# Kernel tuning notes

Measured on AMD Instinct MI355X. Metric: run time of the kernel, lower is better.

Reference implementation:

```python
import jax, jax.numpy as jnp
import numpy as np


def setup_inputs() -> dict:
    key = jax.random.key(0)
    qkv = jax.random.normal(key, (8, 1536, 2048), dtype=jnp.float32)
    return {"qkv": qkv, "n_heads": 8}


def reference(qkv, n_heads):
    # qkv: [N, H*3*C, T] -> output [N, H*C, T]
    bs, width, length = qkv.shape
    assert width % (3 * n_heads) == 0
    ch = width // (3 * n_heads)
    qkv_r = qkv.reshape(bs * n_heads, 3 * ch, length)
    q, k, v = qkv_r[:, :ch], qkv_r[:, ch:2 * ch], qkv_r[:, 2 * ch:]
    scale = 1.0 / np.sqrt(np.sqrt(ch))  # applied to both q and k
    # [B, T, S] scores
    weight = jnp.einsum('bct,bcs->bts', q * scale, k * scale)
    weight = jax.nn.softmax(weight.astype(jnp.float32), axis=-1).astype(weight.dtype)
    a = jnp.einsum('bts,bcs->bct', weight, v)
    return a.reshape(bs, n_heads * ch, length)
```

## Files before the change

kernel.cpp:

```cpp
#include <hip/hip_runtime.h>


typedef __bf16 bf16;
typedef __bf16 bf16x4 __attribute__((ext_vector_type(4)));
typedef __bf16 bf16x8 __attribute__((ext_vector_type(8)));
typedef float  f32x4  __attribute__((ext_vector_type(4)));
typedef float  f32x16 __attribute__((ext_vector_type(16)));
typedef unsigned int u32;

#define NLEN 2048
#define DCH  64
#define HSTR (NLEN * DCH * 2)
#define WS_K (16u * 1024u * 1024u)
#define WS_V (32u * 1024u * 1024u)
#define WS_NEED (48u * 1024u * 1024u)
#define PSCALE 0.42466119f

__device__ __forceinline__ int swzK(int row, int cb) {
    return row * 128 + ((((cb >> 4) ^ row) & 7) << 4) + (cb & 15);
}
__device__ __forceinline__ int swzO(int row, int cb) {
    int g = cb >> 4;
    g = (g & ~7) | ((g ^ row) & 7);
    return row * 512 + (g << 4) + (cb & 15);
}

__device__ __forceinline__ void gload16(const char* g, char* l) {
    __builtin_amdgcn_global_load_lds((const __attribute__((address_space(1))) void*)g,
                                     (__attribute__((address_space(3))) void*)l, 16, 0, 0);
}

__global__ __launch_bounds__(256)
void prep(const float* __restrict__ qkv, char* __restrict__ ws)
{
    const int tid  = threadIdx.x;
    const int pb   = blockIdx.x;
    const int head = blockIdx.y;
    const int type = blockIdx.z;

    const float* src = qkv + (size_t)head * (3 * DCH) * NLEN + (size_t)type * DCH * NLEN;
    char* dst = ws + (type == 0 ? 0u : (type == 1 ? WS_K : WS_V))
                   + (size_t)head * HSTR + (size_t)pb * 8192;

    if (type < 2) {
        __shared__ float T[64][65];
        #pragma unroll
        for (int p = 0; p < 4; ++p) {
            int idx = tid + p * 256;
            int c = idx >> 4, q4 = idx & 15;
            float4 f = *(const float4*)(src + (size_t)c * NLEN + pb * 64 + q4 * 4);
            T[q4 * 4 + 0][c] = f.x * PSCALE;
            T[q4 * 4 + 1][c] = f.y * PSCALE;
            T[q4 * 4 + 2][c] = f.z * PSCALE;
            T[q4 * 4 + 3][c] = f.w * PSCALE;
        }
        __syncthreads();
        #pragma unroll
        for (int p = 0; p < 2; ++p) {
            int gidx = tid + p * 256;
            int s = gidx >> 3, G = gidx & 7;
            int c0 = (G ^ (s & 7)) * 8;
            bf16 tmp[8];
            #pragma unroll
            for (int j = 0; j < 8; ++j) tmp[j] = (bf16)T[s][c0 + j];
            *(bf16x8*)(dst + s * 128 + G * 16) = *(bf16x8*)tmp;
        }
    } else {
        const int c = tid >> 2, so = (tid & 3) * 16;
        const float* sp = src + (size_t)c * NLEN + pb * 64 + so;
        float f[16];
        #pragma unroll
        for (int j = 0; j < 4; ++j) *(f32x4*)(f + 4 * j) = *(const f32x4*)(sp + 4 * j);
        #pragma unroll
        for (int gl = 0; gl < 2; ++gl) {
            bf16 tmp[8];
            #pragma unroll
            for (int j = 0; j < 8; ++j) tmp[j] = (bf16)f[gl * 8 + j];
            const int Gp = ((so >> 3) + gl) ^ (c & 7);
            *(bf16x8*)(dst + c * 128 + Gp * 16) = *(bf16x8*)tmp;
        }
    }
}

__global__ __launch_bounds__(256, 2)
void attn_main(const char* __restrict__ ws, float* __restrict__ out)
{
    const int tid  = threadIdx.x;
    const int lane = tid & 63;
    const int w    = tid >> 6;
    const int hi   = lane >> 5;
    const int ll5  = lane & 31;

    const int bid  = blockIdx.x;
    const int head = (bid & 7) * 8 + ((bid >> 3) & 7);
    const int tblk = bid >> 6;
    const int t0   = tblk * 256;

    const char* Qb = ws + (size_t)head * HSTR + (size_t)t0 * 128;
    const char* Kb = ws + WS_K + (size_t)head * HSTR;
    const char* Vb = ws + WS_V + (size_t)head * HSTR;

    __shared__ __align__(16) char lds[32768];

    #pragma unroll
    for (int i = 0; i < 8; ++i)
        gload16(Qb + tid * 16 + i * 4096, lds + tid * 16 + i * 4096);
    asm volatile("s_waitcnt vmcnt(0)");
    __syncthreads();

    bf16x8 qf0[4], qf1[4];
    #pragma unroll
    for (int kc = 0; kc < 4; ++kc) {
        qf0[kc] = *(const bf16x8*)(lds + swzK(w * 64 + ll5,      kc * 32 + hi * 16));
        qf1[kc] = *(const bf16x8*)(lds + swzK(w * 64 + 32 + ll5, kc * 32 + hi * 16));
    }
    __syncthreads();

    gload16(Kb + tid * 16,        lds + tid * 16);
    gload16(Kb + 4096 + tid * 16, lds + 4096 + tid * 16);
    gload16(Vb + tid * 16,        lds + 8192 + tid * 16);
    gload16(Vb + 4096 + tid * 16, lds + 12288 + tid * 16);
    asm volatile("s_waitcnt vmcnt(0)");
    __syncthreads();

    f32x16 o00 = {}, o01 = {}, o10 = {}, o11 = {};
    float l0 = 0.f, l1 = 0.f;
    int cur = 0;

    for (int sb = 0; sb < 32; ++sb) {
        if (sb < 31) {
            char* bn = lds + (cur ^ 1) * 16384;
            const char* kn = Kb + (size_t)(sb + 1) * 8192;
            const char* vn = Vb + (size_t)(sb + 1) * 8192;
            gload16(kn + tid * 16,        bn + tid * 16);
            gload16(kn + 4096 + tid * 16, bn + 4096 + tid * 16);
            gload16(vn + tid * 16,        bn + 8192 + tid * 16);
            gload16(vn + 4096 + tid * 16, bn + 12288 + tid * 16);
        }
        char* Kc = lds + cur * 16384;
        char* Vc = Kc + 8192;

        f32x16 s00 = {}, s10 = {}, s01 = {}, s11 = {};
        __builtin_amdgcn_s_setprio(1);
        #pragma unroll
        for (int kc = 0; kc < 4; ++kc) {
            bf16x8 a0 = *(const bf16x8*)(Kc + swzK(ll5,      kc * 32 + hi * 16));
            bf16x8 a1 = *(const bf16x8*)(Kc + swzK(32 + ll5, kc * 32 + hi * 16));
            s00 = __builtin_amdgcn_mfma_f32_32x32x16_bf16(a0, qf0[kc], s00, 0, 0, 0);
            s10 = __builtin_amdgcn_mfma_f32_32x32x16_bf16(a1, qf0[kc], s10, 0, 0, 0);
            s01 = __builtin_amdgcn_mfma_f32_32x32x16_bf16(a0, qf1[kc], s01, 0, 0, 0);
            s11 = __builtin_amdgcn_mfma_f32_32x32x16_bf16(a1, qf1[kc], s11, 0, 0, 0);
        }
        __builtin_amdgcn_s_setprio(0);

        {
            float a = 0.f, b = 0.f, c = 0.f, d = 0.f;
            #pragma unroll
            for (int r = 0; r < 16; r += 4) {
                s00[r+0] = __builtin_amdgcn_exp2f(s00[r+0]); a += s00[r+0];
                s00[r+1] = __builtin_amdgcn_exp2f(s00[r+1]); b += s00[r+1];
                s00[r+2] = __builtin_amdgcn_exp2f(s00[r+2]); c += s00[r+2];
                s00[r+3] = __builtin_amdgcn_exp2f(s00[r+3]); d += s00[r+3];
            }
            #pragma unroll
            for (int r = 0; r < 16; r += 4) {
                s10[r+0] = __builtin_amdgcn_exp2f(s10[r+0]); a += s10[r+0];
                s10[r+1] = __builtin_amdgcn_exp2f(s10[r+1]); b += s10[r+1];
                s10[r+2] = __builtin_amdgcn_exp2f(s10[r+2]); c += s10[r+2];
                s10[r+3] = __builtin_amdgcn_exp2f(s10[r+3]); d += s10[r+3];
            }
            l0 += (a + b) + (c + d);
        }
        {
            float a = 0.f, b = 0.f, c = 0.f, d = 0.f;
            #pragma unroll
            for (int r = 0; r < 16; r += 4) {
                s01[r+0] = __builtin_amdgcn_exp2f(s01[r+0]); a += s01[r+0];
                s01[r+1] = __builtin_amdgcn_exp2f(s01[r+1]); b += s01[r+1];
                s01[r+2] = __builtin_amdgcn_exp2f(s01[r+2]); c += s01[r+2];
                s01[r+3] = __builtin_amdgcn_exp2f(s01[r+3]); d += s01[r+3];
            }
            #pragma unroll
            for (int r = 0; r < 16; r += 4) {
                s11[r+0] = __builtin_amdgcn_exp2f(s11[r+0]); a += s11[r+0];
                s11[r+1] = __builtin_amdgcn_exp2f(s11[r+1]); b += s11[r+1];
                s11[r+2] = __builtin_amdgcn_exp2f(s11[r+2]); c += s11[r+2];
                s11[r+3] = __builtin_amdgcn_exp2f(s11[r+3]); d += s11[r+3];
            }
            l1 += (a + b) + (c + d);
        }

        bf16x8 pa0[4], pa1[4];
        #pragma unroll
        for (int th = 0; th < 2; ++th) {
            const f32x16& sl = th ? s01 : s00;
            const f32x16& sh = th ? s11 : s10;
            bf16x8* pa = th ? pa1 : pa0;
            #pragma unroll
            for (int ks = 0; ks < 4; ++ks) {
                const f32x16& pp = (ks < 2) ? sl : sh;
                const int rb = (ks & 1) * 8;
                u32 X, X2, Y, Y2;
                asm("v_cvt_pk_bf16_f32 %0, %1, %2" : "=v"(X)  : "v"(pp[rb + 0]), "v"(pp[rb + 1]));
                asm("v_cvt_pk_bf16_f32 %0, %1, %2" : "=v"(X2) : "v"(pp[rb + 2]), "v"(pp[rb + 3]));
                asm("v_cvt_pk_bf16_f32 %0, %1, %2" : "=v"(Y)  : "v"(pp[rb + 4]), "v"(pp[rb + 5]));
                asm("v_cvt_pk_bf16_f32 %0, %1, %2" : "=v"(Y2) : "v"(pp[rb + 6]), "v"(pp[rb + 7]));
                asm("v_permlane32_swap_b32 %0, %1" : "+v"(X),  "+v"(Y));
                asm("v_permlane32_swap_b32 %0, %1" : "+v"(X2), "+v"(Y2));
                u32 wds[4] = {X, X2, Y, Y2};
                pa[ks] = *(bf16x8*)wds;
            }
        }

        __builtin_amdgcn_s_setprio(1);
        #pragma unroll
        for (int ks = 0; ks < 4; ++ks) {
            bf16x8 b0 = *(const bf16x8*)(Vc + swzK(ll5,      ks * 32 + hi * 16));
            bf16x8 b1 = *(const bf16x8*)(Vc + swzK(32 + ll5, ks * 32 + hi * 16));
            o00 = __builtin_amdgcn_mfma_f32_32x32x16_bf16(pa0[ks], b0, o00, 0, 0, 0);
            o01 = __builtin_amdgcn_mfma_f32_32x32x16_bf16(pa0[ks], b1, o01, 0, 0, 0);
            o10 = __builtin_amdgcn_mfma_f32_32x32x16_bf16(pa1[ks], b0, o10, 0, 0, 0);
            o11 = __builtin_amdgcn_mfma_f32_32x32x16_bf16(pa1[ks], b1, o11, 0, 0, 0);
        }
        __builtin_amdgcn_s_setprio(0);

        asm volatile("s_waitcnt vmcnt(0)");
        __syncthreads();
        cur ^= 1;
    }

    const float lf0 = l0 + __shfl_xor(l0, 32);
    const float lf1 = l1 + __shfl_xor(l1, 32);
    const float li0 = 1.0f / lf0;
    const float li1 = 1.0f / lf1;
    float a0[16], a1[16];
    #pragma unroll
    for (int r = 0; r < 16; ++r) {
        const int src = (r & 3) + 8 * (r >> 2) + 4 * hi;
        a0[r] = __shfl(li0, src);
        a1[r] = __shfl(li1, src);
    }
    #pragma unroll
    for (int r = 0; r < 16; ++r) {
        o00[r] *= a0[r]; o01[r] *= a0[r];
        o10[r] *= a1[r]; o11[r] *= a1[r];
    }

    float* op = out + (size_t)head * DCH * NLEN + t0;
    float* Of = (float*)lds;

    #pragma unroll
    for (int p = 0; p < 2; ++p) {
        __syncthreads();
        if ((w >> 1) == p) {
            const int wl = w & 1;
            #pragma unroll
            for (int th = 0; th < 2; ++th) {
                const f32x16& v0 = th ? o10 : o00;
                const f32x16& v1 = th ? o11 : o01;
                #pragma unroll
                for (int j = 0; j < 4; ++j) {
                    const int tb = wl * 64 + th * 32 + 8 * j + 4 * hi;
                    f32x4 u0, u1;
                    #pragma unroll
                    for (int r = 0; r < 4; ++r) { u0[r] = v0[4 * j + r]; u1[r] = v1[4 * j + r]; }
                    *(f32x4*)((char*)Of + swzO(ll5,      tb * 4)) = u0;
                    *(f32x4*)((char*)Of + swzO(32 + ll5, tb * 4)) = u1;
                }
            }
        }
        __syncthreads();
        #pragma unroll
        for (int ch = 0; ch < 8; ++ch) {
            const int idx = tid + ch * 256;
            const int c = idx >> 5, tq = idx & 31;
            f32x4 v = *(const f32x4*)((char*)Of + swzO(c, tq * 16));
            *(float4*)(op + (size_t)c * NLEN + p * 128 + tq * 4) = *(float4*)&v;
        }
    }
}

#define CEXP_FB 0.18033688011112042f
#define QSCALE_FB 0.35355339059327373f
__global__ __launch_bounds__(512, 2)
void attn_fwd(const float* __restrict__ qkv, float* __restrict__ out)
{
    const int tid  = threadIdx.x;
    const int lane = tid & 63;
    const int w    = tid >> 6;
    const int lg   = lane >> 4;
    const int ll   = lane & 15;
    const int tblk = blockIdx.x;
    const int head = blockIdx.y;
    const int t0   = tblk * 128;

    const float* qp = qkv + (size_t)head * (3 * DCH) * NLEN;
    const float* kp = qp + (size_t)DCH * NLEN;
    const float* vp = kp + (size_t)DCH * NLEN;

    __shared__ __align__(16) char lds[48 * 1024];
    char* Qs = lds;
    char* Ks = lds + 16 * 1024;
    char* Vs = lds + 24 * 1024;
    char* Ps = lds + 32 * 1024 + w * 2048;

    {
        const int G = tid >> 6;
        #pragma unroll
        for (int it = 0; it < 2; ++it) {
            const int t = (tid & 63) + it * 64;
            const float* src = qp + (size_t)(G * 8) * NLEN + t0 + t;
            bf16 tmp[8];
            #pragma unroll
            for (int j = 0; j < 8; ++j) tmp[j] = (bf16)(src[(size_t)j * NLEN] * QSCALE_FB);
            *(bf16x8*)(Qs + swzK(t, G * 16)) = *(bf16x8*)tmp;
        }
    }
    __syncthreads();
    bf16x8 qf[2];
    #pragma unroll
    for (int kk = 0; kk < 2; ++kk)
        qf[kk] = *(const bf16x8*)(Qs + swzK(w * 16 + ll, kk * 64 + lg * 16));

    f32x4 o[4] = {};
    float m_r = -3.0e38f, l_r = 0.f;

    for (int sb = 0; sb < NLEN / 64; ++sb) {
        const int s0 = sb * 64;
        __syncthreads();
        {
            const int s = tid & 63, G = tid >> 6;
            const float* src = kp + (size_t)(G * 8) * NLEN + s0 + s;
            bf16 tmp[8];
            #pragma unroll
            for (int j = 0; j < 8; ++j) tmp[j] = (bf16)(src[(size_t)j * NLEN] * QSCALE_FB);
            *(bf16x8*)(Ks + swzK(s, G * 16)) = *(bf16x8*)tmp;
        }
        {
            const int c = tid >> 3, s8 = tid & 7;
            const float* src = vp + (size_t)c * NLEN + s0 + s8 * 8;
            const float4 f0 = *(const float4*)src;
            const float4 f1 = *(const float4*)(src + 4);
            bf16 tmp[8] = {(bf16)f0.x, (bf16)f0.y, (bf16)f0.z, (bf16)f0.w,
                           (bf16)f1.x, (bf16)f1.y, (bf16)f1.z, (bf16)f1.w};
            *(bf16x8*)(Vs + swzK(c, s8 * 16)) = *(bf16x8*)tmp;
        }
        __syncthreads();

        f32x4 sf[4] = {};
        #pragma unroll
        for (int kk = 0; kk < 2; ++kk)
            #pragma unroll
            for (int fs = 0; fs < 4; ++fs) {
                bf16x8 a = *(const bf16x8*)(Ks + swzK(fs * 16 + ll, kk * 64 + lg * 16));
                sf[fs] = __builtin_amdgcn_mfma_f32_16x16x32_bf16(a, qf[kk], sf[fs], 0, 0, 0);
            }

        float mx;
        {
            f32x4 m4 = sf[0];
            #pragma unroll
            for (int fs = 1; fs < 4; ++fs) {
                m4[0] = fmaxf(m4[0], sf[fs][0]); m4[1] = fmaxf(m4[1], sf[fs][1]);
                m4[2] = fmaxf(m4[2], sf[fs][2]); m4[3] = fmaxf(m4[3], sf[fs][3]);
            }
            mx = fmaxf(fmaxf(m4[0], m4[1]), fmaxf(m4[2], m4[3]));
        }
        mx = fmaxf(mx, __shfl_xor(mx, 16));
        mx = fmaxf(mx, __shfl_xor(mx, 32));
        const float mnew = fmaxf(m_r, mx);
        const float corr = exp2f((m_r - mnew) * 1.4426950408889634f);
        m_r = mnew;
        const float cm = mnew * 1.4426950408889634f;

        float psum = 0.f;
        #pragma unroll
        for (int fs = 0; fs < 4; ++fs) {
            bf16x4 pw;
            #pragma unroll
            for (int r = 0; r < 4; ++r) {
                float p = exp2f(fmaf(sf[fs][r], 1.4426950408889634f, -cm));
                psum += p;
                pw[r] = (bf16)p;
            }
            *(bf16x4*)(Ps + swzK(ll, 32 * fs + 8 * lg)) = pw;
        }
        psum += __shfl_xor(psum, 16);
        psum += __shfl_xor(psum, 32);
        l_r = l_r * corr + psum;

        float corr4[4];
        #pragma unroll
        for (int r = 0; r < 4; ++r) corr4[r] = __shfl(corr, 4 * lg + r);
        #pragma unroll
        for (int cf = 0; cf < 4; ++cf)
            #pragma unroll
            for (int r = 0; r < 4; ++r) o[cf][r] *= corr4[r];

        #pragma unroll
        for (int kk = 0; kk < 2; ++kk) {
            bf16x8 pa = *(const bf16x8*)(Ps + swzK(ll, kk * 64 + lg * 16));
            #pragma unroll
            for (int cf = 0; cf < 4; ++cf) {
                bf16x8 b = *(const bf16x8*)(Vs + swzK(cf * 16 + ll, kk * 64 + lg * 16));
                o[cf] = __builtin_amdgcn_mfma_f32_16x16x32_bf16(pa, b, o[cf], 0, 0, 0);
            }
        }
    }

    __syncthreads();
    const float linv = 1.0f / l_r;
    float linv4[4];
    #pragma unroll
    for (int r = 0; r < 4; ++r) linv4[r] = __shfl(linv, 4 * lg + r);
    float* Of = (float*)lds;
    #pragma unroll
    for (int cf = 0; cf < 4; ++cf) {
        f32x4 ov;
        #pragma unroll
        for (int r = 0; r < 4; ++r) ov[r] = o[cf][r] * linv4[r];
        *(f32x4*)((char*)Of + swzO(cf * 16 + ll, (w * 16 + 4 * lg) * 4)) = ov;
    }
    __syncthreads();
    float* op = out + (size_t)head * DCH * NLEN + t0;
    #pragma unroll
    for (int it = 0; it < 4; ++it) {
        const int idx = tid + it * 512;
        const int c = idx >> 5, tq = idx & 31;
        f32x4 v = *(const f32x4*)((char*)Of + swzO(c, tq * 16));
        *(float4*)(op + (size_t)c * NLEN + tq * 4) = *(float4*)&v;
    }
}

extern "C" void kernel_launch(void* const* d_in, const int* in_sizes, int n_in,
                              void* d_out, int out_size, void* d_ws, size_t ws_size,
                              hipStream_t stream)
{
    const float* qkv = (const float*)d_in[0];
    float* out = (float*)d_out;
    if (ws_size >= (size_t)WS_NEED) {
        char* ws = (char*)d_ws;
        prep<<<dim3(32, 64, 3), 256, 0, stream>>>(qkv, ws);
        attn_main<<<dim3(512), 256, 0, stream>>>(ws, out);
    } else {
        attn_fwd<<<dim3(16, 64), 512, 0, stream>>>(qkv, out);
    }
}
```

Measured before the change: 101.1 us.

## Deepen K/V pipeline to four LDS buffers and interleave softmax with PV MFMAs

The main attention loop now stages two K/V tiles per iteration into a four-slot LDS ring, doubling shared memory to 64KB. This halves the number of barriers and vmcnt waits per key block. Each tile step splits the softmax of the second query half so its exp and convert work can overlap with the first half's PV MFMAs. Blocks sharing a head also start at different key offsets to spread L2/HBM access. The larger LDS footprint may limit occupancy to fewer blocks per CU.

After: 101.1 us. No clear change (-0.1%).

```diff
diff --git a/kernel.cpp b/kernel.cpp
--- a/kernel.cpp
+++ b/kernel.cpp
@@ -82,6 +82,121 @@
     }
 }
 
+__device__ __forceinline__ void stage_kv(const char* Kb, const char* Vb, char* buf,
+                                         int sblk, int tid)
+{
+    const char* kn = Kb + (size_t)sblk * 8192;
+    const char* vn = Vb + (size_t)sblk * 8192;
+    gload16(kn + tid * 16,        buf + tid * 16);
+    gload16(kn + 4096 + tid * 16, buf + 4096 + tid * 16);
+    gload16(vn + tid * 16,        buf + 8192 + tid * 16);
+    gload16(vn + 4096 + tid * 16, buf + 12288 + tid * 16);
+}
+
+__device__ __forceinline__ void tile_step(const char* Kc, const char* Vc,
+    const bf16x8 qf0[4], const bf16x8 qf1[4],
+    f32x16& o00, f32x16& o01, f32x16& o10, f32x16& o11,
+    float& l0, float& l1, int hi, int ll5)
+{
+    f32x16 s00 = {}, s10 = {}, s01 = {}, s11 = {};
+    __builtin_amdgcn_s_setprio(1);
+    #pragma unroll
+    for (int kc = 0; kc < 4; ++kc) {
+        bf16x8 a0 = *(const bf16x8*)(Kc + swzK(ll5,      kc * 32 + hi * 16));
+        bf16x8 a1 = *(const bf16x8*)(Kc + swzK(32 + ll5, kc * 32 + hi * 16));
+        s00 = __builtin_amdgcn_mfma_f32_32x32x16_bf16(a0, qf0[kc], s00, 0, 0, 0);
+        s10 = __builtin_amdgcn_mfma_f32_32x32x16_bf16(a1, qf0[kc], s10, 0, 0, 0);
+        s01 = __builtin_amdgcn_mfma_f32_32x32x16_bf16(a0, qf1[kc], s01, 0, 0, 0);
+        s11 = __builtin_amdgcn_mfma_f32_32x32x16_bf16(a1, qf1[kc], s11, 0, 0, 0);
+    }
+    __builtin_amdgcn_s_setprio(0);
+
+    bf16x8 pa0[4], pa1[4];
+    {
+        float a = 0.f, b = 0.f, c = 0.f, d = 0.f;
+        #pragma unroll
+        for (int r = 0; r < 16; r += 4) {
+            s00[r+0] = __builtin_amdgcn_exp2f(s00[r+0]); a += s00[r+0];
+            s00[r+1] = __builtin_amdgcn_exp2f(s00[r+1]); b += s00[r+1];
+            s00[r+2] = __builtin_amdgcn_exp2f(s00[r+2]); c += s00[r+2];
+            s00[r+3] = __builtin_amdgcn_exp2f(s00[r+3]); d += s00[r+3];
+        }
+        #pragma unroll
+        for (int r = 0; r < 16; r += 4) {
+            s10[r+0] = __builtin_amdgcn_exp2f(s10[r+0]); a += s10[r+0];
+            s10[r+1] = __builtin_amdgcn_exp2f(s10[r+1]); b += s10[r+1];
+            s10[r+2] = __builtin_amdgcn_exp2f(s10[r+2]); c += s10[r+2];
+            s10[r+3] = __builtin_amdgcn_exp2f(s10[r+3]); d += s10[r+3];
+        }
+        l0 += (a + b) + (c + d);
+        #pragma unroll
+        for (int ks = 0; ks < 4; ++ks) {
+            const f32x16& pp = (ks < 2) ? s00 : s10;
+            const int rb = (ks & 1) * 8;
+            u32 X, X2, Y, Y2;
+            asm("v_cvt_pk_bf16_f32 %0, %1, %2" : "=v"(X)  : "v"(pp[rb + 0]), "v"(pp[rb + 1]));
+            asm("v_cvt_pk_bf16_f32 %0, %1, %2" : "=v"(X2) : "v"(pp[rb + 2]), "v"(pp[rb + 3]));
+            asm("v_cvt_pk_bf16_f32 %0, %1, %2" : "=v"(Y)  : "v"(pp[rb + 4]), "v"(pp[rb + 5]));
+            asm("v_cvt_pk_bf16_f32 %0, %1, %2" : "=v"(Y2) : "v"(pp[rb + 6]), "v"(pp[rb + 7]));
+            asm("v_permlane32_swap_b32 %0, %1" : "+v"(X),  "+v"(Y));
+            asm("v_permlane32_swap_b32 %0, %1" : "+v"(X2), "+v"(Y2));
+            u32 wds[4] = {X, X2, Y, Y2};
+            pa0[ks] = *(bf16x8*)wds;
+        }
+    }
+
+    bf16x8 vb0[4], vb1[4];
+    __builtin_amdgcn_s_setprio(1);
+    #pragma unroll
+    for (int ks = 0; ks < 4; ++ks) {
+        vb0[ks] = *(const bf16x8*)(Vc + swzK(ll5,      ks * 32 + hi * 16));
+        vb1[ks] = *(const bf16x8*)(Vc + swzK(32 + ll5, ks * 32 + hi * 16));
+        o00 = __builtin_amdgcn_mfma_f32_32x32x16_bf16(pa0[ks], vb0[ks], o00, 0, 0, 0);
+        o01 = __builtin_amdgcn_mfma_f32_32x32x16_bf16(pa0[ks], vb1[ks], o01, 0, 0, 0);
+    }
+    __builtin_amdgcn_s_setprio(0);
+    {
+        float a = 0.f, b = 0.f, c = 0.f, d = 0.f;
+        #pragma unroll
+        for (int r = 0; r < 16; r += 4) {
+            s01[r+0] = __builtin_amdgcn_exp2f(s01[r+0]); a += s01[r+0];
+            s01[r+1] = __builtin_amdgcn_exp2f(s01[r+1]); b += s01[r+1];
+            s01[r+2] = __builtin_amdgcn_exp2f(s01[r+2]); c += s01[r+2];
+            s01[r+3] = __builtin_amdgcn_exp2f(s01[r+3]); d += s01[r+3];
+        }
+        #pragma unroll
+        for (int r = 0; r < 16; r += 4) {
+            s11[r+0] = __builtin_amdgcn_exp2f(s11[r+0]); a += s11[r+0];
+            s11[r+1] = __builtin_amdgcn_exp2f(s11[r+1]); b += s11[r+1];
+            s11[r+2] = __builtin_amdgcn_exp2f(s11[r+2]); c += s11[r+2];
+            s11[r+3] = __builtin_amdgcn_exp2f(s11[r+3]); d += s11[r+3];
+        }
+        l1 += (a + b) + (c + d);
+        #pragma unroll
+        for (int ks = 0; ks < 4; ++ks) {
+            const f32x16& pp = (ks < 2) ? s01 : s11;
+            const int rb = (ks & 1) * 8;
+            u32 X, X2, Y, Y2;
+            asm("v_cvt_pk_bf16_f32 %0, %1, %2" : "=v"(X)  : "v"(pp[rb + 0]), "v"(pp[rb + 1]));
+            asm("v_cvt_pk_bf16_f32 %0, %1, %2" : "=v"(X2) : "v"(pp[rb + 2]), "v"(pp[rb + 3]));
+            asm("v_cvt_pk_bf16_f32 %0, %1, %2" : "=v"(Y)  : "v"(pp[rb + 4]), "v"(pp[rb + 5]));
+            asm("v_cvt_pk_bf16_f32 %0, %1, %2" : "=v"(Y2) : "v"(pp[rb + 6]), "v"(pp[rb + 7]));
+            asm("v_permlane32_swap_b32 %0, %1" : "+v"(X),  "+v"(Y));
+            asm("v_permlane32_swap_b32 %0, %1" : "+v"(X2), "+v"(Y2));
+            u32 wds[4] = {X, X2, Y, Y2};
+            pa1[ks] = *(bf16x8*)wds;
+        }
+    }
+
+    __builtin_amdgcn_s_setprio(1);
+    #pragma unroll
+    for (int ks = 0; ks < 4; ++ks) {
+        o10 = __builtin_amdgcn_mfma_f32_32x32x16_bf16(pa1[ks], vb0[ks], o10, 0, 0, 0);
+        o11 = __builtin_amdgcn_mfma_f32_32x32x16_bf16(pa1[ks], vb1[ks], o11, 0, 0, 0);
+    }
+    __builtin_amdgcn_s_setprio(0);
+}
+
 __global__ __launch_bounds__(256, 2)
 void attn_main(const char* __restrict__ ws, float* __restrict__ out)
 {
@@ -95,12 +210,13 @@
     const int head = (bid & 7) * 8 + ((bid >> 3) & 7);
     const int tblk = bid >> 6;
     const int t0   = tblk * 256;
+    const int sbase = ((bid >> 3) & 1) * 16;
 
     const char* Qb = ws + (size_t)head * HSTR + (size_t)t0 * 128;
     const char* Kb = ws + WS_K + (size_t)head * HSTR;
     const char* Vb = ws + WS_V + (size_t)head * HSTR;
 
-    __shared__ __align__(16) char lds[32768];
+    __shared__ __align__(16) char lds[65536];
 
     #pragma unroll
     for (int i = 0; i < 8; ++i)
@@ -116,117 +232,31 @@
     }
     __syncthreads();
 
-    gload16(Kb + tid * 16,        lds + tid * 16);
-    gload16(Kb + 4096 + tid * 16, lds + 4096 + tid * 16);
-    gload16(Vb + tid * 16,        lds + 8192 + tid * 16);
-    gload16(Vb + 4096 + tid * 16, lds + 12288 + tid * 16);
+    stage_kv(Kb, Vb, lds,         (0 + sbase) & 31, tid);
+    stage_kv(Kb, Vb, lds + 16384, (1 + sbase) & 31, tid);
     asm volatile("s_waitcnt vmcnt(0)");
     __syncthreads();
 
     f32x16 o00 = {}, o01 = {}, o10 = {}, o11 = {};
     float l0 = 0.f, l1 = 0.f;
-    int cur = 0;
-
-    for (int sb = 0; sb < 32; ++sb) {
-        if (sb < 31) {
-            char* bn = lds + (cur ^ 1) * 16384;
-            const char* kn = Kb + (size_t)(sb + 1) * 8192;
-            const char* vn = Vb + (size_t)(sb + 1) * 8192;
-            gload16(kn + tid * 16,        bn + tid * 16);
-            gload16(kn + 4096 + tid * 16, bn + 4096 + tid * 16);
-            gload16(vn + tid * 16,        bn + 8192 + tid * 16);
-            gload16(vn + 4096 + tid * 16, bn + 12288 + tid * 16);
-        }
-        char* Kc = lds + cur * 16384;
-        char* Vc = Kc + 8192;
-
-        f32x16 s00 = {}, s10 = {}, s01 = {}, s11 = {};
-        __builtin_amdgcn_s_setprio(1);
-        #pragma unroll
-        for (int kc = 0; kc < 4; ++kc) {
-            bf16x8 a0 = *(const bf16x8*)(Kc + swzK(ll5,      kc * 32 + hi * 16));
-            bf16x8 a1 = *(const bf16x8*)(Kc + swzK(32 + ll5, kc * 32 + hi * 16));
-            s00 = __builtin_amdgcn_mfma_f32_32x32x16_bf16(a0, qf0[kc], s00, 0, 0, 0);
-            s10 = __builtin_amdgcn_mfma_f32_32x32x16_bf16(a1, qf0[kc], s10, 0, 0, 0);
-            s01 = __builtin_amdgcn_mfma_f32_32x32x16_bf16(a0, qf1[kc], s01, 0, 0, 0);
-            s11 = __builtin_amdgcn_mfma_f32_32x32x16_bf16(a1, qf1[kc], s11, 0, 0, 0);
-        }
-        __builtin_amdgcn_s_setprio(0);
-
+
+    #pragma unroll 1
+    for (int j = 0; j < 16; ++j) {
+        const int i0 = 2 * j;
+        if (j < 15) {
+            stage_kv(Kb, Vb, lds + ((i0 + 2) & 3) * 16384, (i0 + 2 + sbase) & 31, tid);
+            stage_kv(Kb, Vb, lds + ((i0 + 3) & 3) * 16384, (i0 + 3 + sbase) & 31, tid);
+        }
         {
-            float a = 0.f, b = 0.f, c = 0.f, d = 0.f;
-            #pragma unroll
-            for (int r = 0; r < 16; r += 4) {
-                s00[r+0] = __builtin_amdgcn_exp2f(s00[r+0]); a += s00[r+0];
-                s00[r+1] = __builtin_amdgcn_exp2f(s00[r+1]); b += s00[r+1];
-                s00[r+2] = __builtin_amdgcn_exp2f(s00[r+2]); c += s00[r+2];
-                s00[r+3] = __builtin_amdgcn_exp2f(s00[r+3]); d += s00[r+3];
-            }
-            #pragma unroll
-            for (int r = 0; r < 16; r += 4) {
-                s10[r+0] = __builtin_amdgcn_exp2f(s10[r+0]); a += s10[r+0];
-                s10[r+1] = __builtin_amdgcn_exp2f(s10[r+1]); b += s10[r+1];
-                s10[r+2] = __builtin_amdgcn_exp2f(s10[r+2]); c += s10[r+2];
-                s10[r+3] = __builtin_amdgcn_exp2f(s10[r+3]); d += s10[r+3];
-            }
-            l0 += (a + b) + (c + d);
+            const char* Kc = lds + (i0 & 3) * 16384;
+            tile_step(Kc, Kc + 8192, qf0, qf1, o00, o01, o10, o11, l0, l1, hi, ll5);
         }
         {
-            float a = 0.f, b = 0.f, c = 0.f, d = 0.f;
-            #pragma unroll
-            for (int r = 0; r < 16; r += 4) {
-                s01[r+0] = __builtin_amdgcn_exp2f(s01[r+0]); a += s01[r+0];
-                s01[r+1] = __builtin_amdgcn_exp2f(s01[r+1]); b += s01[r+1];
-                s01[r+2] = __builtin_amdgcn_exp2f(s01[r+2]); c += s01[r+2];
-                s01[r+3] = __builtin_amdgcn_exp2f(s01[r+3]); d += s01[r+3];
-            }
-            #pragma unroll
-            for (int r = 0; r < 16; r += 4) {
-                s11[r+0] = __builtin_amdgcn_exp2f(s11[r+0]); a += s11[r+0];
-                s11[r+1] = __builtin_amdgcn_exp2f(s11[r+1]); b += s11[r+1];
-                s11[r+2] = __builtin_amdgcn_exp2f(s11[r+2]); c += s11[r+2];
-                s11[r+3] = __builtin_amdgcn_exp2f(s11[r+3]); d += s11[r+3];
-            }
-            l1 += (a + b) + (c + d);
-        }
-
-        bf16x8 pa0[4], pa1[4];
-        #pragma unroll
-        for (int th = 0; th < 2; ++th) {
-            const f32x16& sl = th ? s01 : s00;
-            const f32x16& sh = th ? s11 : s10;
-            bf16x8* pa = th ? pa1 : pa0;
-            #pragma unroll
-            for (int ks = 0; ks < 4; ++ks) {
-                const f32x16& pp = (ks < 2) ? sl : sh;
-                const int rb = (ks & 1) * 8;
-                u32 X, X2, Y, Y2;
-                asm("v_cvt_pk_bf16_f32 %0, %1, %2" : "=v"(X)  : "v"(pp[rb + 0]), "v"(pp[rb + 1]));
-                asm("v_cvt_pk_bf16_f32 %0, %1, %2" : "=v"(X2) : "v"(pp[rb + 2]), "v"(pp[rb + 3]));
-                asm("v_cvt_pk_bf16_f32 %0, %1, %2" : "=v"(Y)  : "v"(pp[rb + 4]), "v"(pp[rb + 5]));
-                asm("v_cvt_pk_bf16_f32 %0, %1, %2" : "=v"(Y2) : "v"(pp[rb + 6]), "v"(pp[rb + 7]));
-                asm("v_permlane32_swap_b32 %0, %1" : "+v"(X),  "+v"(Y));
-                asm("v_permlane32_swap_b32 %0, %1" : "+v"(X2), "+v"(Y2));
-                u32 wds[4] = {X, X2, Y, Y2};
-                pa[ks] = *(bf16x8*)wds;
-            }
-        }
-
-        __builtin_amdgcn_s_setprio(1);
-        #pragma unroll
-        for (int ks = 0; ks < 4; ++ks) {
-            bf16x8 b0 = *(const bf16x8*)(Vc + swzK(ll5,      ks * 32 + hi * 16));
-            bf16x8 b1 = *(const bf16x8*)(Vc + swzK(32 + ll5, ks * 32 + hi * 16));
-            o00 = __builtin_amdgcn_mfma_f32_32x32x16_bf16(pa0[ks], b0, o00, 0, 0, 0);
-            o01 = __builtin_amdgcn_mfma_f32_32x32x16_bf16(pa0[ks], b1, o01, 0, 0, 0);
-            o10 = __builtin_amdgcn_mfma_f32_32x32x16_bf16(pa1[ks], b0, o10, 0, 0, 0);
-            o11 = __builtin_amdgcn_mfma_f32_32x32x16_bf16(pa1[ks], b1, o11, 0, 0, 0);
-        }
-        __builtin_amdgcn_s_setprio(0);
-
+            const char* Kc = lds + ((i0 + 1) & 3) * 16384;
+            tile_step(Kc, Kc + 8192, qf0, qf1, o00, o01, o10, o11, l0, l1, hi, ll5);
+        }
         asm volatile("s_waitcnt vmcnt(0)");
         __syncthreads();
-        cur ^= 1;
     }
 
     const float lf0 = l0 + __shfl_xor(l0, 32);
@@ -280,7 +310,6 @@
     }
 }
 
-#define CEXP_FB 0.18033688011112042f
 #define QSCALE_FB 0.35355339059327373f
 __global__ __launch_bounds__(512, 2)
 void attn_fwd(const float* __restrict__ qkv, float* __restrict__ out)
```

## Load K/V fragments directly from global in MFMA layout, dropping LDS staging

Applied to the files above, without the earlier changes.

The preprocessing kernel now writes K and V into a fragment-major layout matching the MFMA operand order, so the main attention loop loads K/V fragments straight from global (L2) into registers instead of staging through double-buffered LDS with barriers. The loop is split into two half-tiles so one exp/convert phase can overlap the other's MFMAs, with the next K tile prefetched into registers. Blocks also stagger their starting key tile to spread L2 traffic. This removes the per-iteration syncthreads and LDS traffic, but each wave now reads K/V redundantly from global/L2 and register pressure rises.

Result: no change. 102.6 us (+1.4%).

```diff
diff --git a/kernel.cpp b/kernel.cpp
--- a/kernel.cpp
+++ b/kernel.cpp
@@ -59,15 +59,24 @@
         for (int p = 0; p < 2; ++p) {
             int gidx = tid + p * 256;
             int s = gidx >> 3, G = gidx & 7;
-            int c0 = (G ^ (s & 7)) * 8;
-            bf16 tmp[8];
-            #pragma unroll
-            for (int j = 0; j < 8; ++j) tmp[j] = (bf16)T[s][c0 + j];
-            *(bf16x8*)(dst + s * 128 + G * 16) = *(bf16x8*)tmp;
+            if (type == 0) {
+                int c0 = (G ^ (s & 7)) * 8;
+                bf16 tmp[8];
+                #pragma unroll
+                for (int j = 0; j < 8; ++j) tmp[j] = (bf16)T[s][c0 + j];
+                *(bf16x8*)(dst + s * 128 + G * 16) = *(bf16x8*)tmp;
+            } else {
+                const int kc = G >> 1, hi = G & 1;
+                bf16 tmp[8];
+                #pragma unroll
+                for (int j = 0; j < 8; ++j) tmp[j] = (bf16)T[s][G * 8 + j];
+                *(bf16x8*)(dst + kc * 2048 + ((s >> 5) & 1) * 1024 + hi * 512
+                               + (s & 31) * 16) = *(bf16x8*)tmp;
+            }
         }
     } else {
-        const int c = tid >> 2, so = (tid & 3) * 16;
-        const float* sp = src + (size_t)c * NLEN + pb * 64 + so;
+        const int c = tid >> 2, m = tid & 3;
+        const float* sp = src + (size_t)c * NLEN + pb * 64 + m * 16;
         float f[16];
         #pragma unroll
         for (int j = 0; j < 4; ++j) *(f32x4*)(f + 4 * j) = *(const f32x4*)(sp + 4 * j);
@@ -76,9 +85,43 @@
             bf16 tmp[8];
             #pragma unroll
             for (int j = 0; j < 8; ++j) tmp[j] = (bf16)f[gl * 8 + j];
-            const int Gp = ((so >> 3) + gl) ^ (c & 7);
-            *(bf16x8*)(dst + c * 128 + Gp * 16) = *(bf16x8*)tmp;
-        }
+            *(bf16x8*)(dst + m * 2048 + ((c >> 5) & 1) * 1024 + gl * 512
+                           + (c & 31) * 16) = *(bf16x8*)tmp;
+        }
+    }
+}
+
+__device__ __forceinline__ void expcvt(f32x16& slo, f32x16& shi, float& l, bf16x8 pa[4])
+{
+    float a = 0.f, b = 0.f, c = 0.f, d = 0.f;
+    #pragma unroll
+    for (int r = 0; r < 16; r += 4) {
+        slo[r+0] = __builtin_amdgcn_exp2f(slo[r+0]); a += slo[r+0];
+        slo[r+1] = __builtin_amdgcn_exp2f(slo[r+1]); b += slo[r+1];
+        slo[r+2] = __builtin_amdgcn_exp2f(slo[r+2]); c += slo[r+2];
+        slo[r+3] = __builtin_amdgcn_exp2f(slo[r+3]); d += slo[r+3];
+    }
+    #pragma unroll
+    for (int r = 0; r < 16; r += 4) {
+        shi[r+0] = __builtin_amdgcn_exp2f(shi[r+0]); a += shi[r+0];
+        shi[r+1] = __builtin_amdgcn_exp2f(shi[r+1]); b += shi[r+1];
+        shi[r+2] = __builtin_amdgcn_exp2f(shi[r+2]); c += shi[r+2];
+        shi[r+3] = __builtin_amdgcn_exp2f(shi[r+3]); d += shi[r+3];
+    }
+    l += (a + b) + (c + d);
+    #pragma unroll
+    for (int ks = 0; ks < 4; ++ks) {
+        const f32x16& pp = (ks < 2) ? slo : shi;
+        const int rb = (ks & 1) * 8;
+        u32 X, X2, Y, Y2;
+        asm("v_cvt_pk_bf16_f32 %0, %1, %2" : "=v"(X)  : "v"(pp[rb + 0]), "v"(pp[rb + 1]));
+        asm("v_cvt_pk_bf16_f32 %0, %1, %2" : "=v"(X2) : "v"(pp[rb + 2]), "v"(pp[rb + 3]));
+        asm("v_cvt_pk_bf16_f32 %0, %1, %2" : "=v"(Y)  : "v"(pp[rb + 4]), "v"(pp[rb + 5]));
+        asm("v_cvt_pk_bf16_f32 %0, %1, %2" : "=v"(Y2) : "v"(pp[rb + 6]), "v"(pp[rb + 7]));
+        asm("v_permlane32_swap_b32 %0, %1" : "+v"(X),  "+v"(Y));
+        asm("v_permlane32_swap_b32 %0, %1" : "+v"(X2), "+v"(Y2));
+        u32 wds[4] = {X, X2, Y, Y2};
+        pa[ks] = *(bf16x8*)wds;
     }
 }
 
@@ -95,6 +138,7 @@
     const int head = (bid & 7) * 8 + ((bid >> 3) & 7);
     const int tblk = bid >> 6;
     const int t0   = tblk * 256;
+    const int sbase = ((bid >> 3) & 1) * 16;
 
     const char* Qb = ws + (size_t)head * HSTR + (size_t)t0 * 128;
     const char* Kb = ws + WS_K + (size_t)head * HSTR;
@@ -114,119 +158,77 @@
         qf0[kc] = *(const bf16x8*)(lds + swzK(w * 64 + ll5,      kc * 32 + hi * 16));
         qf1[kc] = *(const bf16x8*)(lds + swzK(w * 64 + 32 + ll5, kc * 32 + hi * 16));
     }
-    __syncthreads();
-
-    gload16(Kb + tid * 16,        lds + tid * 16);
-    gload16(Kb + 4096 + tid * 16, lds + 4096 + tid * 16);
-    gload16(Vb + tid * 16,        lds + 8192 + tid * 16);
-    gload16(Vb + 4096 + tid * 16, lds + 12288 + tid * 16);
-    asm volatile("s_waitcnt vmcnt(0)");
-    __syncthreads();
+
+    const int voff = hi * 512 + ll5 * 16;
+
+    bf16x8 kf0[4], kf1[4];
+    {
+        const char* Kt = Kb + (size_t)sbase * 8192 + voff;
+        #pragma unroll
+        for (int kc = 0; kc < 4; ++kc) {
+            kf0[kc] = *(const bf16x8*)(Kt + kc * 2048);
+            kf1[kc] = *(const bf16x8*)(Kt + kc * 2048 + 1024);
+        }
+    }
 
     f32x16 o00 = {}, o01 = {}, o10 = {}, o11 = {};
     float l0 = 0.f, l1 = 0.f;
-    int cur = 0;
-
-    for (int sb = 0; sb < 32; ++sb) {
-        if (sb < 31) {
-            char* bn = lds + (cur ^ 1) * 16384;
-            const char* kn = Kb + (size_t)(sb + 1) * 8192;
-            const char* vn = Vb + (size_t)(sb + 1) * 8192;
-            gload16(kn + tid * 16,        bn + tid * 16);
-            gload16(kn + 4096 + tid * 16, bn + 4096 + tid * 16);
-            gload16(vn + tid * 16,        bn + 8192 + tid * 16);
-            gload16(vn + 4096 + tid * 16, bn + 12288 + tid * 16);
-        }
-        char* Kc = lds + cur * 16384;
-        char* Vc = Kc + 8192;
-
-        f32x16 s00 = {}, s10 = {}, s01 = {}, s11 = {};
+
+    #pragma unroll 1
+    for (int i = 0; i < 32; ++i) {
+        const int ti = (i + sbase) & 31;
+
+        bf16x8 vf0[4], vf1[4];
+        {
+            const char* Vt = Vb + (size_t)ti * 8192 + voff;
+            #pragma unroll
+            for (int ks = 0; ks < 4; ++ks) {
+                vf0[ks] = *(const bf16x8*)(Vt + ks * 2048);
+                vf1[ks] = *(const bf16x8*)(Vt + ks * 2048 + 1024);
+            }
+        }
+
+        f32x16 sa = {}, sb = {};
         __builtin_amdgcn_s_setprio(1);
         #pragma unroll
         for (int kc = 0; kc < 4; ++kc) {
-            bf16x8 a0 = *(const bf16x8*)(Kc + swzK(ll5,      kc * 32 + hi * 16));
-            bf16x8 a1 = *(const bf16x8*)(Kc + swzK(32 + ll5, kc * 32 + hi * 16));
-            s00 = __builtin_amdgcn_mfma_f32_32x32x16_bf16(a0, qf0[kc], s00, 0, 0, 0);
-            s10 = __builtin_amdgcn_mfma_f32_32x32x16_bf16(a1, qf0[kc], s10, 0, 0, 0);
-            s01 = __builtin_amdgcn_mfma_f32_32x32x16_bf16(a0, qf1[kc], s01, 0, 0, 0);
-            s11 = __builtin_amdgcn_mfma_f32_32x32x16_bf16(a1, qf1[kc], s11, 0, 0, 0);
+            sa = __builtin_amdgcn_mfma_f32_32x32x16_bf16(kf0[kc], qf0[kc], sa, 0, 0, 0);
+            sb = __builtin_amdgcn_mfma_f32_32x32x16_bf16(kf1[kc], qf0[kc], sb, 0, 0, 0);
         }
         __builtin_amdgcn_s_setprio(0);
-
-        {
-            float a = 0.f, b = 0.f, c = 0.f, d = 0.f;
-            #pragma unroll
-            for (int r = 0; r < 16; r += 4) {
-                s00[r+0] = __builtin_amdgcn_exp2f(s00[r+0]); a += s00[r+0];
-                s00[r+1] = __builtin_amdgcn_exp2f(s00[r+1]); b += s00[r+1];
-                s00[r+2] = __builtin_amdgcn_exp2f(s00[r+2]); c += s00[r+2];
-                s00[r+3] = __builtin_amdgcn_exp2f(s00[r+3]); d += s00[r+3];
-            }
-            #pragma unroll
-            for (int r = 0; r < 16; r += 4) {
-                s10[r+0] = __builtin_amdgcn_exp2f(s10[r+0]); a += s10[r+0];
-                s10[r+1] = __builtin_amdgcn_exp2f(s10[r+1]); b += s10[r+1];
-                s10[r+2] = __builtin_amdgcn_exp2f(s10[r+2]); c += s10[r+2];
-                s10[r+3] = __builtin_amdgcn_exp2f(s10[r+3]); d += s10[r+3];
-            }
-            l0 += (a + b) + (c + d);
-        }
-        {
-            float a = 0.f, b = 0.f, c = 0.f, d = 0.f;
-            #pragma unroll
-            for (int r = 0; r < 16; r += 4) {
-                s01[r+0] = __builtin_amdgcn_exp2f(s01[r+0]); a += s01[r+0];
-                s01[r+1] = __builtin_amdgcn_exp2f(s01[r+1]); b += s01[r+1];
-                s01[r+2] = __builtin_amdgcn_exp2f(s01[r+2]); c += s01[r+2];
-                s01[r+3] = __builtin_amdgcn_exp2f(s01[r+3]); d += s01[r+3];
-            }
-            #pragma unroll
-            for (int r = 0; r < 16; r += 4) {
-                s11[r+0] = __builtin_amdgcn_exp2f(s11[r+0]); a += s11[r+0];
-                s11[r+1] = __builtin_amdgcn_exp2f(s11[r+1]); b += s11[r+1];
-                s11[r+2] = __builtin_amdgcn_exp2f(s11[r+2]); c += s11[r+2];
-                s11[r+3] = __builtin_amdgcn_exp2f(s11[r+3]); d += s11[r+3];
-            }
-            l1 += (a + b) + (c + d);
-        }
-
-        bf16x8 pa0[4], pa1[4];
-        #pragma unroll
-        for (int th = 0; th < 2; ++th) {
-            const f32x16& sl = th ? s01 : s00;
-            const f32x16& sh = th ? s11 : s10;
-            bf16x8* pa = th ? pa1 : pa0;
-            #pragma unroll
-            for (int ks = 0; ks < 4; ++ks) {
-                const f32x16& pp = (ks < 2) ? sl : sh;
-                const int rb = (ks & 1) * 8;
-                u32 X, X2, Y, Y2;
-                asm("v_cvt_pk_bf16_f32 %0, %1, %2" : "=v"(X)  : "v"(pp[rb + 0]), "v"(pp[rb + 1]));
-                asm("v_cvt_pk_bf16_f32 %0, %1, %2" : "=v"(X2) : "v"(pp[rb + 2]), "v"(pp[rb + 3]));
-                asm("v_cvt_pk_bf16_f32 %0, %1, %2" : "=v"(Y)  : "v"(pp[rb + 4]), "v"(pp[rb + 5]));
-                asm("v_cvt_pk_bf16_f32 %0, %1, %2" : "=v"(Y2) : "v"(pp[rb + 6]), "v"(pp[rb + 7]));
-                asm("v_permlane32_swap_b32 %0, %1" : "+v"(X),  "+v"(Y));
-                asm("v_permlane32_swap_b32 %0, %1" : "+v"(X2), "+v"(Y2));
-                u32 wds[4] = {X, X2, Y, Y2};
-                pa[ks] = *(bf16x8*)wds;
-            }
-        }
-
+        bf16x8 pa0[4];
+        expcvt(sa, sb, l0, pa0);
+
+        f32x16 sc = {}, sd = {};
         __builtin_amdgcn_s_setprio(1);
         #pragma unroll
+        for (int kc = 0; kc < 4; ++kc) {
+            sc = __builtin_amdgcn_mfma_f32_32x32x16_bf16(kf0[kc], qf1[kc], sc, 0, 0, 0);
+            sd = __builtin_amdgcn_mfma_f32_32x32x16_bf16(kf1[kc], qf1[kc], sd, 0, 0, 0);
+        }
+        __builtin_amdgcn_s_setprio(0);
+
+        if (i != 31) {
+            const char* Kt = Kb + (size_t)(((i + 1 + sbase) & 31)) * 8192 + voff;
+            #pragma unroll
+            for (int kc = 0; kc < 4; ++kc) {
+                kf0[kc] = *(const bf16x8*)(Kt + kc * 2048);
+                kf1[kc] = *(const bf16x8*)(Kt + kc * 2048 + 1024);
+            }
+        }
+
+        bf16x8 pa1[4];
+        expcvt(sc, sd, l1, pa1);
+
+        __builtin_amdgcn_s_setprio(1);
+        #pragma unroll
         for (int ks = 0; ks < 4; ++ks) {
-            bf16x8 b0 = *(const bf16x8*)(Vc + swzK(ll5,      ks * 32 + hi * 16));
-            bf16x8 b1 = *(const bf16x8*)(Vc + swzK(32 + ll5, ks * 32 + hi * 16));
-            o00 = __builtin_amdgcn_mfma_f32_32x32x16_bf16(pa0[ks], b0, o00, 0, 0, 0);
-            o01 = __builtin_amdgcn_mfma_f32_32x32x16_bf16(pa0[ks], b1, o01, 0, 0, 0);
-            o10 = __builtin_amdgcn_mfma_f32_32x32x16_bf16(pa1[ks], b0, o10, 0, 0, 0);
-            o11 = __builtin_amdgcn_mfma_f32_32x32x16_bf16(pa1[ks], b1, o11, 0, 0, 0);
+            o00 = __builtin_amdgcn_mfma_f32_32x32x16_bf16(pa0[ks], vf0[ks], o00, 0, 0, 0);
+            o01 = __builtin_amdgcn_mfma_f32_32x32x16_bf16(pa0[ks], vf1[ks], o01, 0, 0, 0);
+            o10 = __builtin_amdgcn_mfma_f32_32x32x16_bf16(pa1[ks], vf0[ks], o10, 0, 0, 0);
+            o11 = __builtin_amdgcn_mfma_f32_32x32x16_bf16(pa1[ks], vf1[ks], o11, 0, 0, 0);
         }
         __builtin_amdgcn_s_setprio(0);
-
-        asm volatile("s_waitcnt vmcnt(0)");
-        __syncthreads();
-        cur ^= 1;
     }
 
     const float lf0 = l0 + __shfl_xor(l0, 32);
@@ -280,7 +282,6 @@
     }
 }
 
-#define CEXP_FB 0.18033688011112042f
 #define QSCALE_FB 0.35355339059327373f
 __global__ __launch_bounds__(512, 2)
 void attn_fwd(const float* __restrict__ qkv, float* __restrict__ out)
```
